# Kernel optimization log

Hardware: AMD Instinct MI355X
Metric: run time of the kernel (lower is better)

Reference implementation:

```python
import jax, jax.numpy as jnp
import numpy as np

B, S, D = 512, 64, 2048


def setup_inputs() -> dict:
    key = jax.random.key(0)
    ks = jax.random.split(key, 5)
    return {
        "classical_state": jax.random.normal(ks[0], (B, D), jnp.float32),
        "amplitudes": jax.random.normal(ks[1], (S, D), jnp.float32),
        "phases": jax.random.normal(ks[2], (S, D), jnp.float32),
        "rotation_gates": jax.random.normal(ks[3], (S, 2, 2), jnp.float32),
        "entanglement_matrix": jax.random.normal(ks[4], (S, S), jnp.float32),
    }


def reference(classical_state, amplitudes, phases, rotation_gates, entanglement_matrix):
    # classical_state: [B, D]; amplitudes/phases: [S, D]; rotation_gates: [S, 2, 2]
    b, d = classical_state.shape
    s = amplitudes.shape[0]

    # create_superposition
    norm_amp = amplitudes / jnp.linalg.norm(amplitudes, axis=1, keepdims=True)  # F.normalize p=2 dim=1
    real_amp = norm_amp * (jnp.cos(phases) + jnp.sin(phases))                   # [S, D]

    # _apply_quantum_rotation: per-pair (x[:, 2p:2p+2] @ gate) for each gate i -> vectorized over S and pairs
    xr = classical_state.reshape(b, d // 2, 2)                                  # [B, P, 2]
    rotated = jnp.einsum('bpi,sij->bspj', xr, rotation_gates).reshape(b, s, d)  # [B, S, D]

    states = real_amp[None, :, :] * rotated                                     # weighted superposition [B, S, D]

    # _apply_entanglement: softmax over rows then matmul across superposition dim
    ent_w = jax.nn.softmax(entanglement_matrix, axis=1)                          # [S, S]
    entangled = jnp.einsum('st,btd->bsd', ent_w, states)                         # [B, S, D]

    # collapse_superposition: multinomial over softmax(sum of squares), gather selected state
    logits = jnp.sum(entangled * entangled, axis=2)                              # [B, S]
    probabilities = jax.nn.softmax(logits, axis=1)
    outcome = jax.random.categorical(jax.random.key(42), logits, axis=1)         # [B] ~ multinomial(probabilities)
    collapsed = jnp.take_along_axis(entangled, outcome[:, None, None], axis=1)[:, 0, :]  # [B, D]
    return collapsed
```

## Files before the change

### kernel.cpp

```cpp
#include <hip/hip_runtime.h>
#include <math.h>

#define NB 512
#define NS 64
#define ND 2048
#define NP 1024

__device__ __forceinline__ unsigned rotl32(unsigned x, int d) {
    return (x << d) | (x >> (32 - d));
}

__device__ __forceinline__ void threefry2x32(unsigned k0, unsigned k1,
                                             unsigned& x0, unsigned& x1) {
    const unsigned ks0 = k0, ks1 = k1, ks2 = k0 ^ k1 ^ 0x1BD11BDAu;
    const int r0[4] = {13, 15, 26, 6};
    const int r1[4] = {17, 29, 16, 24};
    x0 += ks0; x1 += ks1;
#pragma unroll
    for (int i = 0; i < 4; ++i) { x0 += x1; x1 = rotl32(x1, r0[i]); x1 ^= x0; }
    x0 += ks1; x1 += ks2 + 1u;
#pragma unroll
    for (int i = 0; i < 4; ++i) { x0 += x1; x1 = rotl32(x1, r1[i]); x1 ^= x0; }
    x0 += ks2; x1 += ks0 + 2u;
#pragma unroll
    for (int i = 0; i < 4; ++i) { x0 += x1; x1 = rotl32(x1, r0[i]); x1 ^= x0; }
    x0 += ks0; x1 += ks1 + 3u;
#pragma unroll
    for (int i = 0; i < 4; ++i) { x0 += x1; x1 = rotl32(x1, r1[i]); x1 ^= x0; }
    x0 += ks1; x1 += ks2 + 4u;
#pragma unroll
    for (int i = 0; i < 4; ++i) { x0 += x1; x1 = rotl32(x1, r0[i]); x1 ^= x0; }
    x0 += ks2; x1 += ks0 + 5u;
}

__global__ void __launch_bounds__(256)
k_MQ(const float* __restrict__ amp, const float* __restrict__ ph,
     const float* __restrict__ G, const float* __restrict__ E,
     float* __restrict__ M0, float* __restrict__ M1, float* __restrict__ Qt) {
    __shared__ float norm2[NS];
    __shared__ float W_l[NS], in_l[NS];
    __shared__ float Gl[NS * 4];
    const int blk = blockIdx.x;
    const int tid = threadIdx.x;
    const int srow = blk >> 2;

    {
        const int r = tid >> 2, sub = tid & 3;
        const float4* a4 = (const float4*)(amp + r * ND);
        float acc = 0.f;
#pragma unroll 8
        for (int i = 0; i < 128; ++i) {
            float4 v = a4[sub + 4 * i];
            acc += v.x * v.x + v.y * v.y + v.z * v.z + v.w * v.w;
        }
        acc += __shfl_xor(acc, 1, 4);
        acc += __shfl_xor(acc, 2, 4);
        if (sub == 0) norm2[r] = acc;
    }
    Gl[tid] = G[tid];
    __syncthreads();
    if (tid < NS) {
        in_l[tid] = 1.0f / sqrtf(norm2[tid]);
        float e = E[srow * NS + tid];
        float m = e;
        for (int off = 32; off; off >>= 1) m = fmaxf(m, __shfl_down(m, off));
        m = __shfl(m, 0);
        float ex = expf(e - m);
        float sum = ex;
        for (int off = 32; off; off >>= 1) sum += __shfl_down(sum, off);
        sum = __shfl(sum, 0);
        W_l[tid] = ex / sum;
    }
    __syncthreads();

    const int p = ((blk & 3) << 8) + tid;
    const float2* a2 = (const float2*)amp;
    const float2* p2 = (const float2*)ph;
    float a0 = 0.f, a1 = 0.f, b0 = 0.f, b1 = 0.f;
#pragma unroll 4
    for (int t = 0; t < NS; ++t) {
        float2 av = a2[t * NP + p];
        float2 pv = p2[t * NP + p];
        float w = W_l[t], in = in_l[t];
        float ra0 = av.x * in * (__cosf(pv.x) + __sinf(pv.x));
        float ra1 = av.y * in * (__cosf(pv.y) + __sinf(pv.y));
        float wr0 = w * ra0, wr1 = w * ra1;
        a0 += wr0 * Gl[4 * t + 0];
        b0 += wr0 * Gl[4 * t + 2];
        a1 += wr1 * Gl[4 * t + 1];
        b1 += wr1 * Gl[4 * t + 3];
    }
    float2 m0v = {a0, a1}, m1v = {b0, b1};
    ((float2*)(M0 + srow * ND))[p] = m0v;
    ((float2*)(M1 + srow * ND))[p] = m1v;
    Qt[(3 * p + 0) * NS + srow] = a0 * a0 + a1 * a1;
    Qt[(3 * p + 1) * NS + srow] = a0 * b0 + a1 * b1;
    Qt[(3 * p + 2) * NS + srow] = b0 * b0 + b1 * b1;
}

__global__ void __launch_bounds__(512)
k_row(const float* __restrict__ x, const float* __restrict__ Qt,
      const float* __restrict__ M0, const float* __restrict__ M1,
      float* __restrict__ out) {
    __shared__ float2 xs[NP];
    __shared__ float part[8][NS];
    __shared__ int o_sh;
    const int b = blockIdx.x;
    const int tid = threadIdx.x;

    ((float4*)xs)[tid] = ((const float4*)(x + b * ND))[tid];
    __syncthreads();

    const int w = tid >> 6, s = tid & 63;
    {
        float acc = 0.f;
        const int p0 = w << 7;
#pragma unroll 4
        for (int p = p0; p < p0 + 128; ++p) {
            float q0 = Qt[(3 * p + 0) * NS + s];
            float q1 = Qt[(3 * p + 1) * NS + s];
            float q2 = Qt[(3 * p + 2) * NS + s];
            float2 v = xs[p];
            acc += v.x * v.x * q0 + 2.f * v.x * v.y * q1 + v.y * v.y * q2;
        }
        part[w][s] = acc;
    }
    __syncthreads();

    if (tid < 64) {
        float l = 0.f;
#pragma unroll
        for (int k = 0; k < 8; ++k) l += part[k][tid];
        unsigned n = (unsigned)(b * NS + tid);
        unsigned t0 = 0u, t1 = n;
        threefry2x32(0u, 42u, t0, t1);
        unsigned bits = t0 ^ t1;
        float u = (float)(bits >> 9) * (1.0f / 8388608.0f);
        u = fmaxf(u, 1.17549435e-38f);
        float g = -logf(-logf(u));
        float best = l + g;
        int bi = tid;
        for (int off = 32; off; off >>= 1) {
            float ov = __shfl_down(best, off);
            int oi = __shfl_down(bi, off);
            if (ov > best || (ov == best && oi < bi)) { best = ov; bi = oi; }
        }
        if (tid == 0) o_sh = bi;
    }
    __syncthreads();

    const int o = o_sh;
    const float2* m0p = (const float2*)(M0 + o * ND);
    const float2* m1p = (const float2*)(M1 + o * ND);
    float2* op = (float2*)(out + b * ND);
#pragma unroll
    for (int k = 0; k < 2; ++k) {
        int p = tid + (k << 9);
        float2 xv = xs[p], m0 = m0p[p], m1 = m1p[p];
        float2 r;
        r.x = xv.x * m0.x + xv.y * m1.x;
        r.y = xv.x * m0.y + xv.y * m1.y;
        op[p] = r;
    }
}

extern "C" void kernel_launch(void* const* d_in, const int* in_sizes, int n_in,
                              void* d_out, int out_size, void* d_ws, size_t ws_size,
                              hipStream_t stream) {
    const float* x   = (const float*)d_in[0];
    const float* amp = (const float*)d_in[1];
    const float* ph  = (const float*)d_in[2];
    const float* G   = (const float*)d_in[3];
    const float* E   = (const float*)d_in[4];
    float* out = (float*)d_out;
    float* ws = (float*)d_ws;

    float* M0 = ws;
    float* M1 = ws + 131072;
    float* Qt = ws + 262144;

    k_MQ <<<256, 256, 0, stream>>>(amp, ph, G, E, M0, M1, Qt);
    k_row<<<512, 512, 0, stream>>>(x, Qt, M0, M1, out);
}
```

Before: 99.07 us.

## Split MQ reduction across 1024 threads and process two batch rows per block

k_MQ now runs 1024 threads per block. The 64-term superposition sum is split into four partial groups of 16, which are combined through shared memory. k_row handles two batch rows per 1024-thread block, so each Qt load is reused for two rows' logits, which halves Qt reads from global/L2. The cost is fewer blocks (256 instead of 512) and an extra shared-memory reduction and sync step in k_MQ.

```diff
diff --git a/kernel.cpp b/kernel.cpp
--- a/kernel.cpp
+++ b/kernel.cpp
@@ -33,31 +33,34 @@
     x0 += ks2; x1 += ks0 + 5u;
 }
 
-__global__ void __launch_bounds__(256)
+__global__ void __launch_bounds__(1024)
 k_MQ(const float* __restrict__ amp, const float* __restrict__ ph,
      const float* __restrict__ G, const float* __restrict__ E,
      float* __restrict__ M0, float* __restrict__ M1, float* __restrict__ Qt) {
     __shared__ float norm2[NS];
     __shared__ float W_l[NS], in_l[NS];
     __shared__ float Gl[NS * 4];
+    __shared__ float4 part4[4][256];
     const int blk = blockIdx.x;
     const int tid = threadIdx.x;
     const int srow = blk >> 2;
 
     {
-        const int r = tid >> 2, sub = tid & 3;
+        const int r = tid >> 4, sub = tid & 15;
         const float4* a4 = (const float4*)(amp + r * ND);
         float acc = 0.f;
 #pragma unroll 8
-        for (int i = 0; i < 128; ++i) {
-            float4 v = a4[sub + 4 * i];
+        for (int i = 0; i < 32; ++i) {
+            float4 v = a4[sub + 16 * i];
             acc += v.x * v.x + v.y * v.y + v.z * v.z + v.w * v.w;
         }
-        acc += __shfl_xor(acc, 1, 4);
-        acc += __shfl_xor(acc, 2, 4);
+        acc += __shfl_down(acc, 8, 16);
+        acc += __shfl_down(acc, 4, 16);
+        acc += __shfl_down(acc, 2, 16);
+        acc += __shfl_down(acc, 1, 16);
         if (sub == 0) norm2[r] = acc;
     }
-    Gl[tid] = G[tid];
+    if (tid < NS * 4) Gl[tid] = G[tid];
     __syncthreads();
     if (tid < NS) {
         in_l[tid] = 1.0f / sqrtf(norm2[tid]);
@@ -73,65 +76,86 @@
     }
     __syncthreads();
 
-    const int p = ((blk & 3) << 8) + tid;
-    const float2* a2 = (const float2*)amp;
-    const float2* p2 = (const float2*)ph;
-    float a0 = 0.f, a1 = 0.f, b0 = 0.f, b1 = 0.f;
+    {
+        const int pi = tid & 255;
+        const int tg = tid >> 8;
+        const int p = ((blk & 3) << 8) + pi;
+        const int t0 = tg << 4;
+        const float2* a2 = (const float2*)amp;
+        const float2* p2 = (const float2*)ph;
+        float a0 = 0.f, a1 = 0.f, b0 = 0.f, b1 = 0.f;
 #pragma unroll 4
-    for (int t = 0; t < NS; ++t) {
-        float2 av = a2[t * NP + p];
-        float2 pv = p2[t * NP + p];
-        float w = W_l[t], in = in_l[t];
-        float ra0 = av.x * in * (__cosf(pv.x) + __sinf(pv.x));
-        float ra1 = av.y * in * (__cosf(pv.y) + __sinf(pv.y));
-        float wr0 = w * ra0, wr1 = w * ra1;
-        a0 += wr0 * Gl[4 * t + 0];
-        b0 += wr0 * Gl[4 * t + 2];
-        a1 += wr1 * Gl[4 * t + 1];
-        b1 += wr1 * Gl[4 * t + 3];
-    }
-    float2 m0v = {a0, a1}, m1v = {b0, b1};
-    ((float2*)(M0 + srow * ND))[p] = m0v;
-    ((float2*)(M1 + srow * ND))[p] = m1v;
-    Qt[(3 * p + 0) * NS + srow] = a0 * a0 + a1 * a1;
-    Qt[(3 * p + 1) * NS + srow] = a0 * b0 + a1 * b1;
-    Qt[(3 * p + 2) * NS + srow] = b0 * b0 + b1 * b1;
-}
-
-__global__ void __launch_bounds__(512)
+        for (int t = t0; t < t0 + 16; ++t) {
+            float2 av = a2[t * NP + p];
+            float2 pv = p2[t * NP + p];
+            float w = W_l[t], in = in_l[t];
+            float ra0 = av.x * in * (__cosf(pv.x) + __sinf(pv.x));
+            float ra1 = av.y * in * (__cosf(pv.y) + __sinf(pv.y));
+            float wr0 = w * ra0, wr1 = w * ra1;
+            a0 += wr0 * Gl[4 * t + 0];
+            b0 += wr0 * Gl[4 * t + 2];
+            a1 += wr1 * Gl[4 * t + 1];
+            b1 += wr1 * Gl[4 * t + 3];
+        }
+        part4[tg][pi] = make_float4(a0, a1, b0, b1);
+    }
+    __syncthreads();
+
+    if (tid < 256) {
+        const int p = ((blk & 3) << 8) + tid;
+        float4 s0 = part4[0][tid], s1 = part4[1][tid],
+               s2 = part4[2][tid], s3 = part4[3][tid];
+        float a0 = s0.x + s1.x + s2.x + s3.x;
+        float a1 = s0.y + s1.y + s2.y + s3.y;
+        float b0 = s0.z + s1.z + s2.z + s3.z;
+        float b1 = s0.w + s1.w + s2.w + s3.w;
+        float2 m0v = {a0, a1}, m1v = {b0, b1};
+        ((float2*)(M0 + srow * ND))[p] = m0v;
+        ((float2*)(M1 + srow * ND))[p] = m1v;
+        Qt[(3 * p + 0) * NS + srow] = a0 * a0 + a1 * a1;
+        Qt[(3 * p + 1) * NS + srow] = a0 * b0 + a1 * b1;
+        Qt[(3 * p + 2) * NS + srow] = b0 * b0 + b1 * b1;
+    }
+}
+
+__global__ void __launch_bounds__(1024)
 k_row(const float* __restrict__ x, const float* __restrict__ Qt,
       const float* __restrict__ M0, const float* __restrict__ M1,
       float* __restrict__ out) {
-    __shared__ float2 xs[NP];
-    __shared__ float part[8][NS];
-    __shared__ int o_sh;
-    const int b = blockIdx.x;
+    __shared__ float2 xs[2 * NP];
+    __shared__ float part[16][2][NS];
+    __shared__ int o_sh[2];
+    const int blk = blockIdx.x;
     const int tid = threadIdx.x;
-
-    ((float4*)xs)[tid] = ((const float4*)(x + b * ND))[tid];
+    const int r0 = 2 * blk;
+
+    ((float4*)xs)[tid] = ((const float4*)(x + r0 * ND))[tid];
     __syncthreads();
 
     const int w = tid >> 6, s = tid & 63;
     {
-        float acc = 0.f;
-        const int p0 = w << 7;
+        float acc0 = 0.f, acc1 = 0.f;
+        const int p0 = w << 6;
 #pragma unroll 4
-        for (int p = p0; p < p0 + 128; ++p) {
+        for (int p = p0; p < p0 + 64; ++p) {
             float q0 = Qt[(3 * p + 0) * NS + s];
             float q1 = Qt[(3 * p + 1) * NS + s];
             float q2 = Qt[(3 * p + 2) * NS + s];
-            float2 v = xs[p];
-            acc += v.x * v.x * q0 + 2.f * v.x * v.y * q1 + v.y * v.y * q2;
-        }
-        part[w][s] = acc;
-    }
-    __syncthreads();
-
-    if (tid < 64) {
+            float2 v0 = xs[p], v1 = xs[NP + p];
+            acc0 += v0.x * v0.x * q0 + 2.f * v0.x * v0.y * q1 + v0.y * v0.y * q2;
+            acc1 += v1.x * v1.x * q0 + 2.f * v1.x * v1.y * q1 + v1.y * v1.y * q2;
+        }
+        part[w][0][s] = acc0;
+        part[w][1][s] = acc1;
+    }
+    __syncthreads();
+
+    if (tid < 128) {
+        const int w2 = tid >> 6;
         float l = 0.f;
 #pragma unroll
-        for (int k = 0; k < 8; ++k) l += part[k][tid];
-        unsigned n = (unsigned)(b * NS + tid);
+        for (int k = 0; k < 16; ++k) l += part[k][w2][s];
+        unsigned n = (unsigned)((r0 + w2) * NS + s);
         unsigned t0 = 0u, t1 = n;
         threefry2x32(0u, 42u, t0, t1);
         unsigned bits = t0 ^ t1;
@@ -139,28 +163,28 @@
         u = fmaxf(u, 1.17549435e-38f);
         float g = -logf(-logf(u));
         float best = l + g;
-        int bi = tid;
+        int bi = s;
         for (int off = 32; off; off >>= 1) {
             float ov = __shfl_down(best, off);
             int oi = __shfl_down(bi, off);
             if (ov > best || (ov == best && oi < bi)) { best = ov; bi = oi; }
         }
-        if (tid == 0) o_sh = bi;
-    }
-    __syncthreads();
-
-    const int o = o_sh;
-    const float2* m0p = (const float2*)(M0 + o * ND);
-    const float2* m1p = (const float2*)(M1 + o * ND);
-    float2* op = (float2*)(out + b * ND);
-#pragma unroll
-    for (int k = 0; k < 2; ++k) {
-        int p = tid + (k << 9);
-        float2 xv = xs[p], m0 = m0p[p], m1 = m1p[p];
-        float2 r;
-        r.x = xv.x * m0.x + xv.y * m1.x;
-        r.y = xv.x * m0.y + xv.y * m1.y;
-        op[p] = r;
+        if (s == 0) o_sh[w2] = bi;
+    }
+    __syncthreads();
+
+#pragma unroll
+    for (int r = 0; r < 2; ++r) {
+        const int o = o_sh[r];
+        const float2* m0p = (const float2*)(M0 + o * ND);
+        const float2* m1p = (const float2*)(M1 + o * ND);
+        const float2* xr = xs + r * NP;
+        float2* op = (float2*)(out + (r0 + r) * ND);
+        float2 xv = xr[tid], m0 = m0p[tid], m1 = m1p[tid];
+        float2 rr;
+        rr.x = xv.x * m0.x + xv.y * m1.x;
+        rr.y = xv.x * m0.y + xv.y * m1.y;
+        op[tid] = rr;
     }
 }
 
@@ -179,6 +203,6 @@
     float* M1 = ws + 131072;
     float* Qt = ws + 262144;
 
-    k_MQ <<<256, 256, 0, stream>>>(amp, ph, G, E, M0, M1, Qt);
-    k_row<<<512, 512, 0, stream>>>(x, Qt, M0, M1, out);
-}
+    k_MQ <<<256, 1024, 0, stream>>>(amp, ph, G, E, M0, M1, Qt);
+    k_row<<<256, 1024, 0, stream>>>(x, Qt, M0, M1, out);
+}
```

After: 90.58 us. 1.09x faster.
